# Performance work log

Hardware: AMD Instinct MI355X
Metric: run time of the kernel (lower is better)

The kernel has to match this reference:

```python
import jax, jax.numpy as jnp
import numpy as np

B, N, F_IN, F_OUT, E = 8, 4096, 256, 256, 131072


def setup_inputs() -> dict:
    key = jax.random.key(0)
    kx, ke, kw = jax.random.split(key, 3)
    x = jax.random.normal(kx, (B, N, F_IN), dtype=jnp.float32)
    edge_index = jax.random.randint(ke, (2, E), 0, N, dtype=jnp.int32)
    # Xavier-uniform init for weight, zeros for bias (matches reset_parameters)
    limit = float(np.sqrt(6.0 / (F_IN + F_OUT)))
    weight = jax.random.uniform(kw, (F_IN, F_OUT), dtype=jnp.float32,
                                minval=-limit, maxval=limit)
    bias = jnp.zeros((F_OUT,), dtype=jnp.float32)
    return {"x": x, "edge_index": edge_index, "weight": weight, "bias": bias}


def reference(x, edge_index, weight, bias):
    # x: (B, N, F_in) -> transformed: (B, N, F_out)
    xt = jnp.einsum("bnf,fo->bno", x, weight)
    n_nodes = x.shape[1]
    # Adjacency is identical for every batch element in the original
    # (built from the same edge_index inside the loop) -> build once.
    # .set(1.0) matches torch's `adj[src, dst] = 1.0` (duplicates collapse).
    adj = jnp.zeros((n_nodes, n_nodes), dtype=xt.dtype)
    adj = adj.at[edge_index[0], edge_index[1]].set(1.0)
    degree = adj.sum(axis=1, keepdims=True) + 1e-6  # (N, 1)
    adj_norm = adj / degree
    # Aggregate: out[b] = adj_norm @ xt[b], batched as one einsum
    out = jnp.einsum("ij,bjf->bif", adj_norm, xt)
    return out + bias
```

## Files before the change

### kernel.cpp

```cpp
#include <hip/hip_runtime.h>
#include <hip/hip_bf16.h>


#define GC_B     8
#define GC_N     4096
#define GC_F     256
#define GC_E     131072
#define GC_M     (GC_B * GC_N)
#define MASK_WPR (GC_N / 32)
#define LIST_CAP 128
#define NPB      32

typedef __attribute__((ext_vector_type(8))) short         short8;
typedef __attribute__((ext_vector_type(2))) float         float2v;
typedef __attribute__((ext_vector_type(4))) float         float4v;
typedef __attribute__((ext_vector_type(4))) unsigned int  uint4v;

static __device__ __forceinline__ unsigned short f2bf_rne(float f) {
    unsigned u = __builtin_bit_cast(unsigned, f);
    u += 0x7fffu + ((u >> 16) & 1u);
    return (unsigned short)(u >> 16);
}

static __device__ __forceinline__ float2v bfpair(unsigned v) {
    return (float2v){__builtin_bit_cast(float, v << 16),
                     __builtin_bit_cast(float, v)};
}

__global__ __launch_bounds__(256) void prep_kernel(
        const float* __restrict__ X, const float* __restrict__ W,
        unsigned short* __restrict__ Xb, unsigned short* __restrict__ Wt,
        unsigned* __restrict__ mask, unsigned* __restrict__ cnt) {
    const int blk = blockIdx.x;
    const int t   = threadIdx.x;
    if (blk < 4096) {
        const size_t i = ((size_t)blk * 256 + t) * 8;
        const float4v v0 = *(const float4v*)(X + i);
        const float4v v1 = *(const float4v*)(X + i + 4);
        union { unsigned short h[8]; short8 s; } u;
        u.h[0] = f2bf_rne(v0[0]); u.h[1] = f2bf_rne(v0[1]);
        u.h[2] = f2bf_rne(v0[2]); u.h[3] = f2bf_rne(v0[3]);
        u.h[4] = f2bf_rne(v1[0]); u.h[5] = f2bf_rne(v1[1]);
        u.h[6] = f2bf_rne(v1[2]); u.h[7] = f2bf_rne(v1[3]);
        *(short8*)(Xb + i) = u.s;
    } else if (blk < 4352) {
        const int n = blk - 4096;
        Wt[n * GC_F + t] = f2bf_rne(W[t * GC_F + n]);
    } else if (blk < 4480) {
        const size_t base = ((size_t)(blk - 4352) * 256 + t) * 4;
        const uint4v z = {0, 0, 0, 0};
        #pragma unroll
        for (int j = 0; j < 4; j++) ((uint4v*)mask)[base + j] = z;
    } else {
        const uint4v z = {0, 0, 0, 0};
        #pragma unroll
        for (int j = 0; j < 4; j++) ((uint4v*)cnt)[(size_t)t * 4 + j] = z;
    }
}

__global__ void build_list_kernel(const int* __restrict__ ei,
                                  unsigned* __restrict__ mask,
                                  unsigned* __restrict__ cnt,
                                  unsigned short* __restrict__ list) {
    const int e = blockIdx.x * blockDim.x + threadIdx.x;
    if (e < GC_E) {
        const int s = ei[e];
        const int d = ei[GC_E + e];
        const unsigned bit = 1u << (d & 31);
        const unsigned old = atomicOr(&mask[s * MASK_WPR + (d >> 5)], bit);
        if (!(old & bit)) {
            const unsigned p = atomicAdd(&cnt[s], 1u);
            if (p < LIST_CAP) list[s * LIST_CAP + p] = (unsigned short)d;
        }
    }
}

__global__ __launch_bounds__(256, 4) void agg_gemm_kernel(
        const unsigned short* __restrict__ Xb, const unsigned* __restrict__ cnt,
        const unsigned short* __restrict__ list,
        const unsigned short* __restrict__ Wt,
        const float* __restrict__ bias, float* __restrict__ out) {
    __shared__ __attribute__((aligned(16))) uint4v lstv[NPB * LIST_CAP / 8];
    __shared__ int degs[NPB];
    __shared__ __attribute__((aligned(16))) uint4v frag[NPB * GC_F / 8];

    const int tid  = threadIdx.x;
    const int w    = tid >> 6;
    const int lane = tid & 63;
    const int b    = blockIdx.x & 7;
    const int n0   = (blockIdx.x >> 3) * NPB;

    {
        const uint4v* src = (const uint4v*)(list + (size_t)n0 * LIST_CAP);
        lstv[tid]       = src[tid];
        lstv[tid + 256] = src[tid + 256];
    }
    if (tid < NPB) {
        const unsigned c = cnt[n0 + tid];
        degs[tid] = (int)(c < LIST_CAP ? c : LIST_CAP);
    }
    __syncthreads();

    const unsigned short* lst = (const unsigned short*)lstv;
    const int fg = lane & 31;
    const int ks = lane >> 5;
    const unsigned short* xbase = Xb + ((size_t)b << 20) + fg * 8;

    #pragma unroll 1
    for (int it = 0; it < 8; ++it) {
        const int t   = w * 8 + it;
        const int deg = degs[t];
        const unsigned short* tl = lst + t * LIST_CAP;

        float2v a0[4] = {}, a1[4] = {}, a2[4] = {}, a3[4] = {};
        int k = ks;
        for (; k + 6 < deg; k += 8) {
            const unsigned o0 = (unsigned)tl[k]     << 8;
            const unsigned o1 = (unsigned)tl[k + 2] << 8;
            const unsigned o2 = (unsigned)tl[k + 4] << 8;
            const unsigned o3 = (unsigned)tl[k + 6] << 8;
            const uint4v v0 = *(const uint4v*)(xbase + o0);
            const uint4v v1 = *(const uint4v*)(xbase + o1);
            const uint4v v2 = *(const uint4v*)(xbase + o2);
            const uint4v v3 = *(const uint4v*)(xbase + o3);
            #pragma unroll
            for (int e = 0; e < 4; e++) {
                a0[e] += bfpair(v0[e]);
                a1[e] += bfpair(v1[e]);
                a2[e] += bfpair(v2[e]);
                a3[e] += bfpair(v3[e]);
            }
        }
        for (; k < deg; k += 2) {
            const uint4v v0 = *(const uint4v*)(xbase + ((unsigned)tl[k] << 8));
            #pragma unroll
            for (int e = 0; e < 4; e++) a0[e] += bfpair(v0[e]);
        }

        float accv[8];
        #pragma unroll
        for (int e = 0; e < 4; e++) {
            const float2v s = (a0[e] + a1[e]) + (a2[e] + a3[e]);
            accv[2 * e]     = s.x;
            accv[2 * e + 1] = s.y;
        }
        #pragma unroll
        for (int e = 0; e < 8; e++)
            accv[e] += __shfl_xor(accv[e], 32, 64);

        if (ks == 0) {
            const float inv = 1.0f / ((float)deg + 1e-6f);
            uint4v o;
            #pragma unroll
            for (int e = 0; e < 4; e++) {
                const float s0 = accv[2 * e] * inv;
                const float s1 = accv[2 * e + 1] * inv;
                o[e] = (unsigned)f2bf_rne(s0) | ((unsigned)f2bf_rne(s1) << 16);
            }
            const int mt = t >> 4, r = t & 15;
            frag[mt * 512 + fg * 16 + (r ^ (fg & 15))] = o;
        }
    }

    const int r     = lane & 15;
    const int q     = lane >> 4;
    const int fbase = w * 64;
    short8 wfr[8];
    {
        const unsigned short* wp = Wt + (size_t)(fbase + r) * GC_F + q * 8;
        #pragma unroll
        for (int kc = 0; kc < 8; kc++) wfr[kc] = *(const short8*)(wp + kc * 32);
    }
    __syncthreads();

    const size_t orow0 = ((size_t)b << 12) + n0;
    const unsigned short* fragb = (const unsigned short*)frag;
    #pragma unroll 1
    for (int ft = 0; ft < 4; ++ft) {
        const int f0 = fbase + ft * 16;
        const float4v bv = *(const float4v*)(bias + f0 + 4 * q);
        #pragma unroll
        for (int mt = 0; mt < 2; mt++) {
            short8 afr[8];
            #pragma unroll
            for (int kc = 0; kc < 8; kc++) {
                const int ch = 4 * kc + q;
                afr[kc] = *(const short8*)(fragb + mt * 4096 + ch * 128 +
                                           (r ^ (ch & 15)) * 8);
            }
            float4v acc = {0, 0, 0, 0};
            #pragma unroll
            for (int kc = 0; kc < 8; kc++)
                acc = __builtin_amdgcn_mfma_f32_16x16x32_bf16(
                    wfr[kc], afr[kc], acc, 0, 0, 0);
            const float4v res = acc + bv;
            __builtin_nontemporal_store(res,
                (float4v*)(out + (orow0 + mt * 16 + r) * GC_F + f0 + 4 * q));
        }
        if (ft < 3) {
            const unsigned short* wp = Wt + (size_t)(f0 + 16 + r) * GC_F + q * 8;
            #pragma unroll
            for (int kc = 0; kc < 8; kc++) wfr[kc] = *(const short8*)(wp + kc * 32);
        }
    }
}

extern "C" void kernel_launch(void* const* d_in, const int* in_sizes, int n_in,
                              void* d_out, int out_size, void* d_ws, size_t ws_size,
                              hipStream_t stream) {
    const float* x      = (const float*)d_in[0];
    const int*   ei     = (const int*)d_in[1];
    const float* weight = (const float*)d_in[2];
    const float* bias   = (const float*)d_in[3];
    float*       out    = (float*)d_out;

    char* p = (char*)d_ws;
    unsigned short* Xb   = (unsigned short*)p;             p += (size_t)GC_M * GC_F * 2;
    unsigned short* Wt   = (unsigned short*)p;             p += (size_t)GC_F * GC_F * 2;
    unsigned*       mask = (unsigned*)p;                   p += (size_t)GC_N * MASK_WPR * 4;
    unsigned*       cnt  = (unsigned*)p;                   p += (size_t)GC_N * 4;
    unsigned short* list = (unsigned short*)p;

    prep_kernel<<<4481, 256, 0, stream>>>(x, weight, Xb, Wt, mask, cnt);

    build_list_kernel<<<(GC_E + 255) / 256, 256, 0, stream>>>(ei, mask, cnt, list);

    agg_gemm_kernel<<<GC_B * (GC_N / NPB), 256, 0, stream>>>(
        Xb, cnt, list, Wt, bias, out);
}
```

Measured before the change: 147.4 us.

## Halve nodes per block and read neighbor lists as packed 128-bit words

Reduces nodes per block from 32 to 16, which doubles the grid and halves shared-memory use per block so more blocks fit per CU, at the cost of reloading the W fragments twice as often. The gather loop now reads four neighbor-index pairs with one 128-bit LDS load and pulls out each lane's index by shift and mask, replacing separate 16-bit LDS loads. The MFMA stage handles a single 16-row tile per block.

```diff
diff --git a/kernel.cpp b/kernel.cpp
--- a/kernel.cpp
+++ b/kernel.cpp
@@ -9,7 +9,7 @@
 #define GC_M     (GC_B * GC_N)
 #define MASK_WPR (GC_N / 32)
 #define LIST_CAP 128
-#define NPB      32
+#define NPB      16
 
 typedef __attribute__((ext_vector_type(8))) short         short8;
 typedef __attribute__((ext_vector_type(2))) float         float2v;
@@ -90,35 +90,35 @@
     const int b    = blockIdx.x & 7;
     const int n0   = (blockIdx.x >> 3) * NPB;
 
-    {
-        const uint4v* src = (const uint4v*)(list + (size_t)n0 * LIST_CAP);
-        lstv[tid]       = src[tid];
-        lstv[tid + 256] = src[tid + 256];
-    }
+    lstv[tid] = ((const uint4v*)(list + (size_t)n0 * LIST_CAP))[tid];
     if (tid < NPB) {
         const unsigned c = cnt[n0 + tid];
         degs[tid] = (int)(c < LIST_CAP ? c : LIST_CAP);
     }
     __syncthreads();
 
-    const unsigned short* lst = (const unsigned short*)lstv;
     const int fg = lane & 31;
     const int ks = lane >> 5;
+    const unsigned sh = (unsigned)ks << 4;
     const unsigned short* xbase = Xb + ((size_t)b << 20) + fg * 8;
 
     #pragma unroll 1
-    for (int it = 0; it < 8; ++it) {
-        const int t   = w * 8 + it;
+    for (int it = 0; it < NPB / 4; ++it) {
+        const int t   = w * 4 + it;
         const int deg = degs[t];
-        const unsigned short* tl = lst + t * LIST_CAP;
+        const uint4v* tlv = &lstv[t * (LIST_CAP / 8)];
+
+        const int nj = (deg + 1 - ks) >> 1;
+        const int G  = nj >> 2;
 
         float2v a0[4] = {}, a1[4] = {}, a2[4] = {}, a3[4] = {};
-        int k = ks;
-        for (; k + 6 < deg; k += 8) {
-            const unsigned o0 = (unsigned)tl[k]     << 8;
-            const unsigned o1 = (unsigned)tl[k + 2] << 8;
-            const unsigned o2 = (unsigned)tl[k + 4] << 8;
-            const unsigned o3 = (unsigned)tl[k + 6] << 8;
+        #pragma unroll 1
+        for (int g = 0; g < G; ++g) {
+            const uint4v lw = tlv[g];
+            const unsigned o0 = ((lw[0] >> sh) & 0xffffu) << 8;
+            const unsigned o1 = ((lw[1] >> sh) & 0xffffu) << 8;
+            const unsigned o2 = ((lw[2] >> sh) & 0xffffu) << 8;
+            const unsigned o3 = ((lw[3] >> sh) & 0xffffu) << 8;
             const uint4v v0 = *(const uint4v*)(xbase + o0);
             const uint4v v1 = *(const uint4v*)(xbase + o1);
             const uint4v v2 = *(const uint4v*)(xbase + o2);
@@ -131,8 +131,10 @@
                 a3[e] += bfpair(v3[e]);
             }
         }
-        for (; k < deg; k += 2) {
-            const uint4v v0 = *(const uint4v*)(xbase + ((unsigned)tl[k] << 8));
+        for (int j = 4 * G; j < nj; ++j) {
+            const unsigned wj = ((const unsigned*)tlv)[j];
+            const uint4v v0 =
+                *(const uint4v*)(xbase + (((wj >> sh) & 0xffffu) << 8));
             #pragma unroll
             for (int e = 0; e < 4; e++) a0[e] += bfpair(v0[e]);
         }
@@ -157,8 +159,7 @@
                 const float s1 = accv[2 * e + 1] * inv;
                 o[e] = (unsigned)f2bf_rne(s0) | ((unsigned)f2bf_rne(s1) << 16);
             }
-            const int mt = t >> 4, r = t & 15;
-            frag[mt * 512 + fg * 16 + (r ^ (fg & 15))] = o;
+            frag[fg * 16 + (t ^ (fg & 15))] = o;
         }
     }
 
@@ -179,24 +180,20 @@
     for (int ft = 0; ft < 4; ++ft) {
         const int f0 = fbase + ft * 16;
         const float4v bv = *(const float4v*)(bias + f0 + 4 * q);
-        #pragma unroll
-        for (int mt = 0; mt < 2; mt++) {
-            short8 afr[8];
-            #pragma unroll
-            for (int kc = 0; kc < 8; kc++) {
-                const int ch = 4 * kc + q;
-                afr[kc] = *(const short8*)(fragb + mt * 4096 + ch * 128 +
-                                           (r ^ (ch & 15)) * 8);
-            }
-            float4v acc = {0, 0, 0, 0};
-            #pragma unroll
-            for (int kc = 0; kc < 8; kc++)
-                acc = __builtin_amdgcn_mfma_f32_16x16x32_bf16(
-                    wfr[kc], afr[kc], acc, 0, 0, 0);
-            const float4v res = acc + bv;
-            __builtin_nontemporal_store(res,
-                (float4v*)(out + (orow0 + mt * 16 + r) * GC_F + f0 + 4 * q));
-        }
+        short8 afr[8];
+        #pragma unroll
+        for (int kc = 0; kc < 8; kc++) {
+            const int ch = 4 * kc + q;
+            afr[kc] = *(const short8*)(fragb + ch * 128 + (r ^ (ch & 15)) * 8);
+        }
+        float4v acc = {0, 0, 0, 0};
+        #pragma unroll
+        for (int kc = 0; kc < 8; kc++)
+            acc = __builtin_amdgcn_mfma_f32_16x16x32_bf16(
+                wfr[kc], afr[kc], acc, 0, 0, 0);
+        const float4v res = acc + bv;
+        __builtin_nontemporal_store(res,
+            (float4v*)(out + (orow0 + r) * GC_F + f0 + 4 * q));
         if (ft < 3) {
             const unsigned short* wp = Wt + (size_t)(f0 + 16 + r) * GC_F + q * 8;
             #pragma unroll
```

Result: slower. 159.3 us (+8.0%).
